# Kernel optimization log

Measured on AMD Instinct MI355X. Metric: run time of the kernel, lower is better.

Reference implementation:

```python
import jax, jax.numpy as jnp
import numpy as np

N = 16384  # n_nodes
D = 64     # feature dim


def setup_inputs() -> dict:
    key = jax.random.key(0)
    kx, ka = jax.random.split(key)
    x = jax.random.normal(kx, (N, D), dtype=jnp.float32)
    # original code only tests adj[idx] == 1, so 0/1 int entries are faithful
    adj = jax.random.randint(ka, (N, N), 0, 2, dtype=jnp.int32)
    return {"x": x, "adj": adj}


def reference(x, adj):
    # GraphPool: for each node, sum its own feature vector plus the feature
    # vectors of all neighbors j with adj[i, j] == 1.
    # Vectorized: out = adj @ x + x  (dense binary SpMM + self term).
    a = (adj == 1).astype(x.dtype)  # [N, N]
    return jnp.matmul(a, x) + x     # [N, D]
```

## Files before the change

### kernel.cpp

```cpp
#include <hip/hip_runtime.h>

#define NN 16384
#define DD 64
#define SPLIT 32
#define KQ (NN / SPLIT)
#define NCH (KQ / 128)

typedef _Float16 f16x8 __attribute__((ext_vector_type(8)));
typedef short    s16x8 __attribute__((ext_vector_type(8)));
typedef float    f32x4 __attribute__((ext_vector_type(4)));
typedef int      i32x4 __attribute__((ext_vector_type(4)));
typedef int      i32x2 __attribute__((ext_vector_type(2)));
typedef unsigned u32;
typedef unsigned long long u64;

__global__ __launch_bounds__(256) void prep_x(const float* __restrict__ x,
                                              _Float16* __restrict__ ws) {
    __shared__ float sx[32][65];
    const int tid = threadIdx.x;
    const int t   = blockIdx.x;
    {
        int r  = tid >> 3;
        int c8 = (tid & 7) * 8;
        const float* src = x + ((size_t)t * 32 + r) * DD + c8;
        f32x4 a = *(const f32x4*)src;
        f32x4 b = *(const f32x4*)(src + 4);
#pragma unroll
        for (int j = 0; j < 4; ++j) { sx[r][c8 + j] = a[j]; sx[r][c8 + 4 + j] = b[j]; }
    }
    __syncthreads();
    const int l = tid & 63;
    const int c = tid >> 6;
    const int q = l >> 4;
    const int m = l & 15;
    f16x8 v;
#pragma unroll
    for (int j = 0; j < 8; ++j)
        v[j] = (_Float16)sx[q * 8 + j][c * 16 + m];
    *(f16x8*)(ws + (((size_t)t * 256 + c * 64 + l) * 8)) = v;
}

__global__ __launch_bounds__(256, 2) void graphpool_gemm(const int* __restrict__ adj,
                                                         const _Float16* __restrict__ xs,
                                                         float* __restrict__ part) {
    __shared__ _Float16 sB[NCH][8192];

    const int tid = threadIdx.x;
    const int w   = tid >> 6;
    const int l   = tid & 63;
    const int q   = l >> 4;
    const int m   = l & 15;

    const int rb    = blockIdx.x >> 5;
    const int kq    = blockIdx.x & 31;
    const int row16 = rb * 64 + w * 16;

#pragma unroll
    for (int n = 0; n < NCH; ++n) {
        const f16x8* src = (const f16x8*)xs + ((size_t)(kq * NCH + n)) * 1024;
        f16x8 t0 = src[tid], t1 = src[256 + tid], t2 = src[512 + tid], t3 = src[768 + tid];
        f16x8* dst = (f16x8*)sB[n];
        dst[tid] = t0; dst[256 + tid] = t1; dst[512 + tid] = t2; dst[768 + tid] = t3;
    }
    __syncthreads();

    const int* abase = adj + (size_t)row16 * NN + (size_t)kq * KQ;

    f32x4 acc[4];
#pragma unroll
    for (int c = 0; c < 4; ++c) acc[c] = (f32x4){0.f, 0.f, 0.f, 0.f};

    i32x2 areg[2][16];

    auto loadAdj = [&](int n, int buf) {
#pragma unroll
        for (int rr = 0; rr < 16; ++rr)
            areg[buf][rr] = ((const i32x2*)(abase + (size_t)rr * NN + n * 128))[l];
    };

    loadAdj(0, 0);
    loadAdj(1, 1);

#pragma unroll
    for (int n = 0; n < NCH; ++n) {
        const int buf = n & 1;

        u32 mine = 0;
#pragma unroll
        for (int rr = 0; rr < 16; ++rr) {
            u64 b0 = __ballot(areg[buf][rr].x != 0);
            u64 b1 = __ballot(areg[buf][rr].y != 0);
            u32 sa = (l & 1) ? (u32)(b0 >> 32) : (u32)b0;
            u32 sb = (l & 1) ? (u32)(b1 >> 32) : (u32)b1;
            u32 sel = (l & 2) ? sb : sa;
            if ((l >> 2) == rr) mine = sel;
        }

        if (n + 2 < NCH) loadAdj(n + 2, buf);

        i32x4 rowAi;
#pragma unroll
        for (int d = 0; d < 4; ++d)
            rowAi[d] = __builtin_amdgcn_ds_bpermute(((m << 2) | d) << 2, (int)mine);

#pragma unroll
        for (int s = 0; s < 4; ++s) {
            const u32 bq = 16 * (s & 1) + 4 * q;
            const u32 dE = (u32)rowAi[s >> 1];
            const u32 dO = (u32)rowAi[2 + (s >> 1)];
            s16x8 ai;
#pragma unroll
            for (int j = 0; j < 8; ++j) {
                u32 dd = (j & 1) ? dO : dE;
                ai[j] = ((dd >> (bq + (j >> 1))) & 1u) ? (short)0x3C00 : (short)0;
            }
            f16x8 af = __builtin_bit_cast(f16x8, ai);
#pragma unroll
            for (int c = 0; c < 4; ++c) {
                f16x8 bf = *(const f16x8*)&sB[n][((s * 4 + c) * 64 + l) * 8];
                acc[c] = __builtin_amdgcn_mfma_f32_16x16x32_f16(af, bf, acc[c], 0, 0, 0);
            }
        }
    }

    float* po = part + (size_t)kq * NN * DD;
#pragma unroll
    for (int c = 0; c < 4; ++c) {
#pragma unroll
        for (int r = 0; r < 4; ++r) {
            size_t off = (size_t)(row16 + q * 4 + r) * DD + c * 16 + m;
            po[off] = acc[c][r];
        }
    }
}

__global__ __launch_bounds__(256) void reduce_add(const float* __restrict__ part,
                                                  const float* __restrict__ x,
                                                  float* __restrict__ out) {
    size_t i = (size_t)blockIdx.x * 256 + threadIdx.x;
    f32x4 v = ((const f32x4*)x)[i];
#pragma unroll
    for (int g = 0; g < SPLIT; ++g)
        v += ((const f32x4*)(part + (size_t)g * NN * DD))[i];
    ((f32x4*)out)[i] = v;
}

__global__ void graphpool_fallback(const int* __restrict__ adj,
                                   const float* __restrict__ x,
                                   float* __restrict__ out) {
    int i = blockIdx.x;
    int d = threadIdx.x;
    float acc = x[(size_t)i * DD + d];
    const int* row = adj + (size_t)i * NN;
    for (int j = 0; j < NN; ++j)
        if (row[j]) acc += x[(size_t)j * DD + d];
    out[(size_t)i * DD + d] = acc;
}

extern "C" void kernel_launch(void* const* d_in, const int* in_sizes, int n_in,
                              void* d_out, int out_size, void* d_ws, size_t ws_size,
                              hipStream_t stream) {
    const float* x   = (const float*)d_in[0];
    const int*   adj = (const int*)d_in[1];
    float*       out = (float*)d_out;

    const size_t xs_bytes   = (size_t)NN * DD * sizeof(_Float16);
    const size_t part_bytes = (size_t)SPLIT * NN * DD * sizeof(float);
    if (ws_size >= xs_bytes + part_bytes) {
        _Float16* xs   = (_Float16*)d_ws;
        float*    part = (float*)((char*)d_ws + xs_bytes);
        prep_x<<<512, 256, 0, stream>>>(x, xs);
        graphpool_gemm<<<256 * SPLIT, 256, 0, stream>>>(adj, xs, part);
        reduce_add<<<1024, 256, 0, stream>>>(part, x, out);
    } else {
        graphpool_fallback<<<NN, 64, 0, stream>>>(adj, x, out);
    }
}
```

Before: 1.363 ms.

## Load adjacency as 16-byte vectors per pair of chunks and repack bitmasks

Adjacency rows are now fetched as int4 (16 bytes per lane) covering two 128-column chunks at once instead of int2 per chunk, halving the number of global load instructions. The ballot/bit-packing scheme is rewritten to build two 32-bit masks per lane and exchange them with bpermute, with the A-fragment bit mapping adjusted to match. Prefetching becomes a simple one-pair-ahead scheme, which reduces the load depth in flight compared with the previous two-chunk double buffer.

```diff
diff --git a/kernel.cpp b/kernel.cpp
--- a/kernel.cpp
+++ b/kernel.cpp
@@ -5,12 +5,12 @@
 #define SPLIT 32
 #define KQ (NN / SPLIT)
 #define NCH (KQ / 128)
+#define NPAIR (KQ / 256)
 
 typedef _Float16 f16x8 __attribute__((ext_vector_type(8)));
 typedef short    s16x8 __attribute__((ext_vector_type(8)));
 typedef float    f32x4 __attribute__((ext_vector_type(4)));
 typedef int      i32x4 __attribute__((ext_vector_type(4)));
-typedef int      i32x2 __attribute__((ext_vector_type(2)));
 typedef unsigned u32;
 typedef unsigned long long u64;
 
@@ -70,58 +70,87 @@
 #pragma unroll
     for (int c = 0; c < 4; ++c) acc[c] = (f32x4){0.f, 0.f, 0.f, 0.f};
 
-    i32x2 areg[2][16];
-
-    auto loadAdj = [&](int n, int buf) {
+    i32x4 areg[16];
+
+    auto loadPair = [&](int p) {
 #pragma unroll
         for (int rr = 0; rr < 16; ++rr)
-            areg[buf][rr] = ((const i32x2*)(abase + (size_t)rr * NN + n * 128))[l];
-    };
-
-    loadAdj(0, 0);
-    loadAdj(1, 1);
-
-#pragma unroll
-    for (int n = 0; n < NCH; ++n) {
-        const int buf = n & 1;
-
-        u32 mine = 0;
+            areg[rr] = ((const i32x4*)(abase + (size_t)rr * NN + p * 256))[l];
+    };
+
+    u32 m0, m1;
+    auto packPair = [&]() {
+        u32 r0 = 0, r1 = 0;
+        const bool selE1 = ((l >> 4) & 1) != 0;
+        const bool selE2 = ((l >> 4) & 2) != 0;
 #pragma unroll
         for (int rr = 0; rr < 16; ++rr) {
-            u64 b0 = __ballot(areg[buf][rr].x != 0);
-            u64 b1 = __ballot(areg[buf][rr].y != 0);
-            u32 sa = (l & 1) ? (u32)(b0 >> 32) : (u32)b0;
-            u32 sb = (l & 1) ? (u32)(b1 >> 32) : (u32)b1;
-            u32 sel = (l & 2) ? sb : sa;
-            if ((l >> 2) == rr) mine = sel;
-        }
-
-        if (n + 2 < NCH) loadAdj(n + 2, buf);
-
-        i32x4 rowAi;
-#pragma unroll
-        for (int d = 0; d < 4; ++d)
-            rowAi[d] = __builtin_amdgcn_ds_bpermute(((m << 2) | d) << 2, (int)mine);
-
+            const i32x4 v = areg[rr];
+            const u64 b0 = __ballot(v.x != 0);
+            const u64 b1 = __ballot(v.y != 0);
+            const u64 b2 = __ballot(v.z != 0);
+            const u64 b3 = __ballot(v.w != 0);
+            const u32 loA = selE1 ? (u32)b1 : (u32)b0;
+            const u32 loB = selE1 ? (u32)b3 : (u32)b2;
+            const u32 loS = selE2 ? loB : loA;
+            const u32 hiA = selE1 ? (u32)(b1 >> 32) : (u32)(b0 >> 32);
+            const u32 hiB = selE1 ? (u32)(b3 >> 32) : (u32)(b2 >> 32);
+            const u32 hiS = selE2 ? hiB : hiA;
+            const bool own = ((l & 15) == rr);
+            r0 = own ? loS : r0;
+            r1 = own ? hiS : r1;
+        }
+        m0 = r0; m1 = r1;
+    };
+
+    auto doChunk = [&](int ci, u32 D0, u32 D1, u32 D2, u32 D3) {
 #pragma unroll
         for (int s = 0; s < 4; ++s) {
-            const u32 bq = 16 * (s & 1) + 4 * q;
-            const u32 dE = (u32)rowAi[s >> 1];
-            const u32 dO = (u32)rowAi[2 + (s >> 1)];
+            const u32 bb = 8 * s + 2 * q;
             s16x8 ai;
-#pragma unroll
-            for (int j = 0; j < 8; ++j) {
-                u32 dd = (j & 1) ? dO : dE;
-                ai[j] = ((dd >> (bq + (j >> 1))) & 1u) ? (short)0x3C00 : (short)0;
-            }
+            ai[0] = ((D0 >> bb) & 1u)       ? (short)0x3C00 : (short)0;
+            ai[1] = ((D1 >> bb) & 1u)       ? (short)0x3C00 : (short)0;
+            ai[2] = ((D2 >> bb) & 1u)       ? (short)0x3C00 : (short)0;
+            ai[3] = ((D3 >> bb) & 1u)       ? (short)0x3C00 : (short)0;
+            ai[4] = ((D0 >> (bb + 1)) & 1u) ? (short)0x3C00 : (short)0;
+            ai[5] = ((D1 >> (bb + 1)) & 1u) ? (short)0x3C00 : (short)0;
+            ai[6] = ((D2 >> (bb + 1)) & 1u) ? (short)0x3C00 : (short)0;
+            ai[7] = ((D3 >> (bb + 1)) & 1u) ? (short)0x3C00 : (short)0;
             f16x8 af = __builtin_bit_cast(f16x8, ai);
 #pragma unroll
             for (int c = 0; c < 4; ++c) {
-                f16x8 bf = *(const f16x8*)&sB[n][((s * 4 + c) * 64 + l) * 8];
+                f16x8 bf = *(const f16x8*)&sB[ci][((s * 4 + c) * 64 + l) * 8];
                 acc[c] = __builtin_amdgcn_mfma_f32_16x16x32_f16(af, bf, acc[c], 0, 0, 0);
             }
         }
-    }
+    };
+
+    auto exchDo = [&](int pairBase, u32 mh0, u32 mh1) {
+        int rA0, rA1, rA2, rA3;
+#pragma unroll
+        for (int e = 0; e < 4; ++e) {
+            int v = __builtin_amdgcn_ds_bpermute(((e << 4) | m) << 2, (int)mh0);
+            if (e == 0) rA0 = v; else if (e == 1) rA1 = v;
+            else if (e == 2) rA2 = v; else rA3 = v;
+        }
+        doChunk(pairBase, (u32)rA0, (u32)rA1, (u32)rA2, (u32)rA3);
+#pragma unroll
+        for (int e = 0; e < 4; ++e) {
+            int v = __builtin_amdgcn_ds_bpermute(((e << 4) | m) << 2, (int)mh1);
+            if (e == 0) rA0 = v; else if (e == 1) rA1 = v;
+            else if (e == 2) rA2 = v; else rA3 = v;
+        }
+        doChunk(pairBase + 1, (u32)rA0, (u32)rA1, (u32)rA2, (u32)rA3);
+    };
+
+    loadPair(0);
+    packPair();
+    u32 p0m0 = m0, p0m1 = m1;
+    loadPair(1);
+    exchDo(0, p0m0, p0m1);
+
+    packPair();
+    exchDo(2, m0, m1);
 
     float* po = part + (size_t)kq * NN * DD;
 #pragma unroll
```

New measurement: 1.371 ms. No clear change (+0.6%).
